# Performance work log

Measured on AMD Instinct MI355X. Metric: run time of the kernel, lower is better.

Reference implementation:

```python
import jax, jax.numpy as jnp
import numpy as np

N_NODES = 100000
N_EDGES = 1600000
IN_CH = 128
HID = 128
OUT_CH = 10
NUM_LAYERS = 3
NUM_GRAPHS = 512


def _glorot(key, shape):
    fan_in, fan_out = shape[0], shape[1]
    lim = jnp.sqrt(6.0 / (fan_in + fan_out))
    return jax.random.uniform(key, shape, jnp.float32, -lim, lim)


def setup_inputs() -> dict:
    key = jax.random.key(0)
    ks = jax.random.split(key, 20)
    inp = {}
    inp["x"] = jax.random.normal(ks[0], (N_NODES, IN_CH), jnp.float32)
    inp["edge_index"] = jax.random.randint(ks[1], (2, N_EDGES), 0, N_NODES, jnp.int64)
    inp["batch"] = jnp.sort(jax.random.randint(ks[2], (N_NODES,), 0, NUM_GRAPHS, jnp.int64))
    # GIN layer MLP params: Linear(in, hid) -> ReLU -> Linear(hid, hid)
    kidx = 3
    for l in range(NUM_LAYERS):
        d_in = IN_CH if l == 0 else HID
        inp[f"w1_{l}"] = _glorot(ks[kidx], (d_in, HID)); kidx += 1
        inp[f"b1_{l}"] = jnp.zeros((HID,), jnp.float32)
        inp[f"w2_{l}"] = _glorot(ks[kidx], (HID, HID)); kidx += 1
        inp[f"b2_{l}"] = jnp.zeros((HID,), jnp.float32)
    inp["lin_w"] = _glorot(ks[kidx], (HID, OUT_CH))
    inp["lin_b"] = jnp.zeros((OUT_CH,), jnp.float32)
    return inp


def _gin_forward(x, src, dst, batch, layer_params, lin_w, lin_b):
    h = x
    n_layers = len(layer_params)
    for i, (w1, b1, w2, b2) in enumerate(layer_params):
        # GINConv: (1 + eps) * h + sum_{j in N(i)} h_j, eps = 0
        agg = jax.ops.segment_sum(h[src], dst, num_segments=N_NODES)
        z = h + agg
        # MLP: Linear -> ReLU -> Linear
        h = jnp.maximum(z @ w1 + b1, 0.0) @ w2 + b2
        if i < n_layers - 1:  # inter-layer ReLU (PyG BasicGNN act)
            h = jnp.maximum(h, 0.0)
    # global_add_pool over batch ids -> [NUM_GRAPHS, HID]
    pooled = jax.ops.segment_sum(h, batch, num_segments=NUM_GRAPHS)
    # dropout(p=0.5) is identity in eval mode
    return pooled @ lin_w + lin_b


def reference(x, edge_index, batch,
              w1_0, b1_0, w2_0, b2_0,
              w1_1, b1_1, w2_1, b2_1,
              w1_2, b1_2, w2_2, b2_2,
              lin_w, lin_b):
    src, dst = edge_index[0], edge_index[1]
    layer_params = [(w1_0, b1_0, w2_0, b2_0),
                    (w1_1, b1_1, w2_1, b2_1),
                    (w1_2, b1_2, w2_2, b2_2)]
    return _gin_forward(x, src, dst, batch, layer_params, lin_w, lin_b)
```

## Files before the change

### kernel.cpp

```cpp
#include <hip/hip_runtime.h>

#define CH 128
#define OUTC 10
#define NB 256
#define BCAP 10240
#define PCHUNK 2048
#define PROWS 128

typedef __attribute__((ext_vector_type(8))) short short8;
typedef __attribute__((ext_vector_type(4))) float f32x4;


__device__ inline unsigned short f2bf(float f) {
    unsigned u = __builtin_bit_cast(unsigned, f);
    u += 0x7fffu + ((u >> 16) & 1u);
    return (unsigned short)(u >> 16);
}
__device__ inline float bflo(unsigned u) { return __builtin_bit_cast(float, u << 16); }
__device__ inline float bfhi(unsigned u) { return __builtin_bit_cast(float, u & 0xffff0000u); }

__device__ inline void acc8(float* a, const uint4& v) {
    a[0] += bflo(v.x); a[1] += bfhi(v.x);
    a[2] += bflo(v.y); a[3] += bfhi(v.y);
    a[4] += bflo(v.z); a[5] += bfhi(v.z);
    a[6] += bflo(v.w); a[7] += bfhi(v.w);
}


__global__ void convert_x_kernel(const float4* __restrict__ x4, uint2* __restrict__ xb, int n4) {
    int i = blockIdx.x * 256 + threadIdx.x;
    if (i < n4) {
        float4 v = x4[i];
        uint2 o;
        o.x = (unsigned)f2bf(v.x) | ((unsigned)f2bf(v.y) << 16);
        o.y = (unsigned)f2bf(v.z) | ((unsigned)f2bf(v.w) << 16);
        xb[i] = o;
    }
}


struct WPtrs { const float* s[6]; unsigned short* d[6]; };

__global__ void transpose_w_kernel(WPtrs p) {
    int m = blockIdx.y;
    int i = blockIdx.x * 256 + threadIdx.x;
    int k = i >> 7;
    int nn = i & 127;
    p.d[m][nn * CH + k] = f2bf(p.s[m][i]);
}


__global__ void partition_kernel(const int* __restrict__ src, const int* __restrict__ dst,
                                 int* __restrict__ bucketCnt, unsigned* __restrict__ pairs, int E) {
    __shared__ int hist[NB];
    __shared__ int base[NB];
    __shared__ int cur[NB];
    int tid = threadIdx.x;
    int e0 = blockIdx.x * PCHUNK;

    hist[tid] = 0;
    __syncthreads();
    #pragma unroll
    for (int i = 0; i < PCHUNK / 256; ++i) {
        int e = e0 + tid + i * 256;
        if (e < E) atomicAdd(&hist[dst[e] >> 9], 1);
    }
    __syncthreads();
    {
        int c = hist[tid];
        base[tid] = (c > 0) ? atomicAdd(&bucketCnt[tid], c) : 0;
        cur[tid] = 0;
    }
    __syncthreads();
    #pragma unroll
    for (int i = 0; i < PCHUNK / 256; ++i) {
        int e = e0 + tid + i * 256;
        if (e < E) {
            int d = dst[e];
            int bkt = d >> 9;
            int p = base[bkt] + atomicAdd(&cur[bkt], 1);
            if (p < BCAP)
                pairs[bkt * BCAP + p] = ((unsigned)(d & 511) << 17) | (unsigned)src[e];
        }
    }
}

__global__ void scan_buckets_kernel(const int* __restrict__ cnt, int* __restrict__ base) {
    __shared__ int sm[NB];
    int tid = threadIdx.x;
    sm[tid] = cnt[tid];
    __syncthreads();
    for (int off = 1; off < NB; off <<= 1) {
        int t = (tid >= off) ? sm[tid - off] : 0;
        __syncthreads();
        sm[tid] += t;
        __syncthreads();
    }
    base[tid] = sm[tid] - cnt[tid];
}


__launch_bounds__(256)
__global__ void build_csr_kernel(const unsigned* __restrict__ pairs, const int* __restrict__ bucketCnt,
                                 const int* __restrict__ bucketBase,
                                 int* __restrict__ offs, int* __restrict__ csr, int N) {
    __shared__ int ldeg[512];
    __shared__ int s0[512], s1[512];
    __shared__ int lexc[512];
    __shared__ int lcur[512];
    __shared__ int lcsr[BCAP];

    int b = blockIdx.x;
    int node0 = b << 9;
    if (node0 >= N) return;
    int nLocal = min(512, N - node0);
    int cnt = min(bucketCnt[b], BCAP);
    int gbase = bucketBase[b];
    int tid = threadIdx.x;

    for (int i = tid; i < 512; i += 256) ldeg[i] = 0;
    __syncthreads();
    for (int i = tid; i < cnt; i += 256)
        atomicAdd(&ldeg[pairs[b * BCAP + i] >> 17], 1);
    __syncthreads();

    for (int i = tid; i < 512; i += 256) s0[i] = ldeg[i];
    __syncthreads();
    int* sp = s0; int* dp = s1;
    for (int off = 1; off < 512; off <<= 1) {
        for (int i = tid; i < 512; i += 256)
            dp[i] = sp[i] + ((i >= off) ? sp[i - off] : 0);
        __syncthreads();
        int* t = sp; sp = dp; dp = t;
    }
    for (int i = tid; i < 512; i += 256) {
        int ex = sp[i] - ldeg[i];
        lexc[i] = ex;
        lcur[i] = ex;
    }
    __syncthreads();

    for (int i = tid; i < cnt; i += 256) {
        unsigned w = pairs[b * BCAP + i];
        int p = atomicAdd(&lcur[w >> 17], 1);
        lcsr[p] = (int)(w & 0x1ffffu);
    }
    __syncthreads();

    for (int i = tid; i < cnt; i += 256) csr[gbase + i] = lcsr[i];
    for (int i = tid; i < nLocal; i += 256) offs[node0 + i] = gbase + lexc[i];
    if (tid == 0 && node0 + nLocal == N) offs[N] = gbase + cnt;
}


template <int L>
__global__ void aggregate_kernel(const uint4* __restrict__ h4, const int* __restrict__ offs,
                                 const int* __restrict__ csr, uint4* __restrict__ z4, int n) {
    int node = blockIdx.x * 16 + (threadIdx.x >> 4);
    int lane = threadIdx.x & 15;
    if (node >= n) return;
    int beg = offs[node], end = offs[node + 1];

    float a[8];
    {
        uint4 self = h4[node * 16 + lane];
        a[0] = bflo(self.x); a[1] = bfhi(self.x);
        a[2] = bflo(self.y); a[3] = bfhi(self.y);
        a[4] = bflo(self.z); a[5] = bfhi(self.z);
        a[6] = bflo(self.w); a[7] = bfhi(self.w);
    }
    int e = beg;
    for (; e + 4 <= end; e += 4) {
        int s0 = csr[e], s1 = csr[e + 1], s2 = csr[e + 2], s3 = csr[e + 3];
        uint4 v0 = h4[s0 * 16 + lane];
        uint4 v1 = h4[s1 * 16 + lane];
        uint4 v2 = h4[s2 * 16 + lane];
        uint4 v3 = h4[s3 * 16 + lane];
        acc8(a, v0); acc8(a, v1); acc8(a, v2); acc8(a, v3);
    }
    for (; e < end; ++e) {
        uint4 v = h4[csr[e] * 16 + lane];
        acc8(a, v);
    }
    uint4 o;
    o.x = (unsigned)f2bf(a[0]) | ((unsigned)f2bf(a[1]) << 16);
    o.y = (unsigned)f2bf(a[2]) | ((unsigned)f2bf(a[3]) << 16);
    o.z = (unsigned)f2bf(a[4]) | ((unsigned)f2bf(a[5]) << 16);
    o.w = (unsigned)f2bf(a[6]) | ((unsigned)f2bf(a[7]) << 16);
    z4[node * 16 + lane] = o;
}


#define PQ 136
#define BM 128

template <int L>
__launch_bounds__(512, 2)
__global__ void mlp_mfma_kernel(const unsigned short* __restrict__ z,
                                const unsigned short* __restrict__ w1t, const float* __restrict__ b1,
                                const unsigned short* __restrict__ w2t, const float* __restrict__ b2,
                                unsigned short* __restrict__ hout, int n, int relu_out) {
    __shared__ __align__(16) unsigned short zs[BM * PQ];
    __shared__ __align__(16) unsigned short ws[CH * PQ];

    int tid = threadIdx.x;
    int row0 = blockIdx.x * BM;
    int wv = tid >> 6;
    int lane = tid & 63;
    int lm = lane & 15;
    int lq = lane >> 4;

    for (int i = tid; i < BM * 16; i += 512) {
        int r = i >> 4, c = i & 15;
        int row = row0 + r;
        uint4 v = (row < n) ? ((const uint4*)z)[row * 16 + c] : make_uint4(0, 0, 0, 0);
        *(uint4*)((char*)zs + r * (PQ * 2) + c * 16) = v;
    }
    for (int i = tid; i < CH * 16; i += 512) {
        int r = i >> 4, c = i & 15;
        *(uint4*)((char*)ws + r * (PQ * 2) + c * 16) = ((const uint4*)w1t)[i];
    }
    __syncthreads();

    f32x4 acc[8];
    #pragma unroll
    for (int nt = 0; nt < 8; ++nt) {
        float bv = b1[nt * 16 + lm];
        acc[nt] = (f32x4){bv, bv, bv, bv};
    }
    int arow = wv * 16 + lm;
    #pragma unroll
    for (int kb = 0; kb < CH; kb += 32) {
        short8 afr = *(const short8*)&zs[arow * PQ + kb + 8 * lq];
        #pragma unroll
        for (int nt = 0; nt < 8; ++nt) {
            short8 bfr = *(const short8*)&ws[(nt * 16 + lm) * PQ + kb + 8 * lq];
            acc[nt] = __builtin_amdgcn_mfma_f32_16x16x32_bf16(afr, bfr, acc[nt], 0, 0, 0);
        }
    }
    __syncthreads();

    #pragma unroll
    for (int nt = 0; nt < 8; ++nt)
        #pragma unroll
        for (int r = 0; r < 4; ++r) {
            float v = fmaxf(acc[nt][r], 0.f);
            zs[(wv * 16 + lq * 4 + r) * PQ + nt * 16 + lm] = f2bf(v);
        }
    for (int i = tid; i < CH * 16; i += 512) {
        int r = i >> 4, c = i & 15;
        *(uint4*)((char*)ws + r * (PQ * 2) + c * 16) = ((const uint4*)w2t)[i];
    }
    __syncthreads();

    #pragma unroll
    for (int nt = 0; nt < 8; ++nt) {
        float bv = b2[nt * 16 + lm];
        acc[nt] = (f32x4){bv, bv, bv, bv};
    }
    #pragma unroll
    for (int kb = 0; kb < CH; kb += 32) {
        short8 afr = *(const short8*)&zs[arow * PQ + kb + 8 * lq];
        #pragma unroll
        for (int nt = 0; nt < 8; ++nt) {
            short8 bfr = *(const short8*)&ws[(nt * 16 + lm) * PQ + kb + 8 * lq];
            acc[nt] = __builtin_amdgcn_mfma_f32_16x16x32_bf16(afr, bfr, acc[nt], 0, 0, 0);
        }
    }
    __syncthreads();

    #pragma unroll
    for (int nt = 0; nt < 8; ++nt)
        #pragma unroll
        for (int r = 0; r < 4; ++r) {
            float v = acc[nt][r];
            if (relu_out) v = fmaxf(v, 0.f);
            zs[(wv * 16 + lq * 4 + r) * PQ + nt * 16 + lm] = f2bf(v);
        }
    __syncthreads();

    for (int i = tid; i < BM * 16; i += 512) {
        int r = i >> 4, c = i & 15;
        int row = row0 + r;
        if (row < n)
            ((uint4*)hout)[row * 16 + c] = *(const uint4*)((char*)zs + r * (PQ * 2) + c * 16);
    }
}


__global__ void pool_partial_kernel(const unsigned* __restrict__ h2, const int* __restrict__ batch,
                                    float* __restrict__ pooled, int n) {
    int r0 = blockIdx.x * PROWS;
    int tid = threadIdx.x;
    int c2 = tid & 63;
    int rs = tid >> 6;
    float a0 = 0.f, a1 = 0.f;
    int prevg = -1;
    #pragma unroll 4
    for (int i = 0; i < PROWS / 4; ++i) {
        int r = r0 + rs + i * 4;
        if (r >= n) break;
        int g = batch[r];
        if (g != prevg) {
            if (prevg >= 0) {
                atomicAdd(&pooled[prevg * CH + 2 * c2], a0);
                atomicAdd(&pooled[prevg * CH + 2 * c2 + 1], a1);
            }
            prevg = g; a0 = 0.f; a1 = 0.f;
        }
        unsigned v = h2[r * 64 + c2];
        a0 += bflo(v); a1 += bfhi(v);
    }
    if (prevg >= 0) {
        atomicAdd(&pooled[prevg * CH + 2 * c2], a0);
        atomicAdd(&pooled[prevg * CH + 2 * c2 + 1], a1);
    }
}

__global__ void final_linear_kernel(const float* __restrict__ pooled, const float* __restrict__ lin_w,
                                    const float* __restrict__ lin_b, float* __restrict__ out) {
    int g = blockIdx.x;
    int tid = threadIdx.x;
    __shared__ float pl[CH];
    pl[tid] = pooled[g * CH + tid];
    __syncthreads();
    if (tid < OUTC) {
        float a = lin_b[tid];
        #pragma unroll 16
        for (int c = 0; c < CH; ++c) a = fmaf(pl[c], lin_w[c * OUTC + tid], a);
        out[g * OUTC + tid] = a;
    }
}


static inline size_t aln(size_t x) { return (x + 255) & ~size_t(255); }

extern "C" void kernel_launch(void* const* d_in, const int* in_sizes, int n_in,
                              void* d_out, int out_size, void* d_ws, size_t ws_size,
                              hipStream_t stream) {
    const float* x      = (const float*)d_in[0];
    const int*   ei     = (const int*)d_in[1];
    const int*   batch  = (const int*)d_in[2];
    const float* w1[3]  = {(const float*)d_in[3], (const float*)d_in[7],  (const float*)d_in[11]};
    const float* b1[3]  = {(const float*)d_in[4], (const float*)d_in[8],  (const float*)d_in[12]};
    const float* w2[3]  = {(const float*)d_in[5], (const float*)d_in[9],  (const float*)d_in[13]};
    const float* b2[3]  = {(const float*)d_in[6], (const float*)d_in[10], (const float*)d_in[14]};
    const float* lin_w  = (const float*)d_in[15];
    const float* lin_b  = (const float*)d_in[16];
    float* out = (float*)d_out;

    int E = in_sizes[1] / 2;
    int N = in_sizes[2];
    int n_graphs = out_size / OUTC;
    const int* src = ei;
    const int* dst = ei + E;

    char* p = (char*)d_ws;
    int* bucketCnt  = (int*)p; p += aln(NB * 4);
    int* bucketBase = (int*)p; p += aln(NB * 4);
    unsigned* pairs = (unsigned*)p; p += aln((size_t)NB * BCAP * 4);
    int* offs       = (int*)p; p += aln((size_t)(N + 1) * 4);
    int* csr        = (int*)p; p += aln((size_t)E * 4);
    unsigned short* xb = (unsigned short*)p; p += aln((size_t)N * CH * 2);
    unsigned short* zb = (unsigned short*)p; p += aln((size_t)N * CH * 2);
    unsigned short* hA = (unsigned short*)p; p += aln((size_t)N * CH * 2);
    unsigned short* hB = (unsigned short*)p; p += aln((size_t)N * CH * 2);
    float* pooled = (float*)p; p += aln((size_t)n_graphs * CH * 4);
    unsigned short* wt[6];
    for (int i = 0; i < 6; ++i) { wt[i] = (unsigned short*)p; p += aln((size_t)CH * CH * 2); }
    (void)ws_size; (void)n_in;

    convert_x_kernel<<<(N * CH / 4 + 255) / 256, 256, 0, stream>>>((const float4*)x, (uint2*)xb, N * CH / 4);
    WPtrs wp;
    for (int l = 0; l < 3; ++l) {
        wp.s[2 * l] = w1[l];     wp.d[2 * l] = wt[2 * l];
        wp.s[2 * l + 1] = w2[l]; wp.d[2 * l + 1] = wt[2 * l + 1];
    }
    transpose_w_kernel<<<dim3(64, 6), 256, 0, stream>>>(wp);

    hipMemsetAsync(bucketCnt, 0, NB * 4, stream);
    partition_kernel<<<(E + PCHUNK - 1) / PCHUNK, 256, 0, stream>>>(src, dst, bucketCnt, pairs, E);
    scan_buckets_kernel<<<1, NB, 0, stream>>>(bucketCnt, bucketBase);
    build_csr_kernel<<<NB, 256, 0, stream>>>(pairs, bucketCnt, bucketBase, offs, csr, N);

    int ablk = (N + 15) / 16;
    int mblk = (N + BM - 1) / BM;

    aggregate_kernel<0><<<ablk, 256, 0, stream>>>((const uint4*)xb, offs, csr, (uint4*)zb, N);
    mlp_mfma_kernel<0><<<mblk, 512, 0, stream>>>(zb, wt[0], b1[0], wt[1], b2[0], hA, N, 1);
    aggregate_kernel<1><<<ablk, 256, 0, stream>>>((const uint4*)hA, offs, csr, (uint4*)zb, N);
    mlp_mfma_kernel<1><<<mblk, 512, 0, stream>>>(zb, wt[2], b1[1], wt[3], b2[1], hB, N, 1);
    aggregate_kernel<2><<<ablk, 256, 0, stream>>>((const uint4*)hB, offs, csr, (uint4*)zb, N);
    mlp_mfma_kernel<2><<<mblk, 512, 0, stream>>>(zb, wt[4], b1[2], wt[5], b2[2], hA, N, 0);

    hipMemsetAsync(pooled, 0, (size_t)n_graphs * CH * 4, stream);
    pool_partial_kernel<<<(N + PROWS - 1) / PROWS, 256, 0, stream>>>(
        (const unsigned*)hA, batch, pooled, N);
    final_linear_kernel<<<n_graphs, CH, 0, stream>>>(pooled, lin_w, lin_b, out);
}
```

Before: 456.0 us.

## Fuse prep kernels, bucket scan into CSR build, pooling into last MLP

Merges the x conversion and weight transpose into one launch, folds the bucket prefix scan into every build_csr block, and fuses global add pooling into the final MLP kernel so the last hidden state is never written out or re-read. It also unrolls the aggregation gather loop to 8 neighbours with a 2-wide tail and adds launch bounds for occupancy. The aim is fewer kernel launches and less global memory traffic. The cost is a redundant 256-entry scan in each CSR block and possibly higher register pressure in the aggregate kernel.

```diff
diff --git a/kernel.cpp b/kernel.cpp
--- a/kernel.cpp
+++ b/kernel.cpp
@@ -5,7 +5,6 @@
 #define NB 256
 #define BCAP 10240
 #define PCHUNK 2048
-#define PROWS 128
 
 typedef __attribute__((ext_vector_type(8))) short short8;
 typedef __attribute__((ext_vector_type(4))) float f32x4;
@@ -27,26 +26,28 @@
 }
 
 
-__global__ void convert_x_kernel(const float4* __restrict__ x4, uint2* __restrict__ xb, int n4) {
-    int i = blockIdx.x * 256 + threadIdx.x;
-    if (i < n4) {
-        float4 v = x4[i];
-        uint2 o;
-        o.x = (unsigned)f2bf(v.x) | ((unsigned)f2bf(v.y) << 16);
-        o.y = (unsigned)f2bf(v.z) | ((unsigned)f2bf(v.w) << 16);
-        xb[i] = o;
-    }
-}
-
-
 struct WPtrs { const float* s[6]; unsigned short* d[6]; };
 
-__global__ void transpose_w_kernel(WPtrs p) {
-    int m = blockIdx.y;
-    int i = blockIdx.x * 256 + threadIdx.x;
-    int k = i >> 7;
-    int nn = i & 127;
-    p.d[m][nn * CH + k] = f2bf(p.s[m][i]);
+__global__ void prep_kernel(const float4* __restrict__ x4, uint2* __restrict__ xb, int n4,
+                            int nConvBlk, WPtrs p) {
+    int tid = threadIdx.x;
+    if ((int)blockIdx.x < nConvBlk) {
+        int i = blockIdx.x * 256 + tid;
+        if (i < n4) {
+            float4 v = x4[i];
+            uint2 o;
+            o.x = (unsigned)f2bf(v.x) | ((unsigned)f2bf(v.y) << 16);
+            o.y = (unsigned)f2bf(v.z) | ((unsigned)f2bf(v.w) << 16);
+            xb[i] = o;
+        }
+    } else {
+        int b = blockIdx.x - nConvBlk;
+        int m = b >> 6;
+        int i = (b & 63) * 256 + tid;
+        int k = i >> 7;
+        int nn = i & 127;
+        p.d[m][nn * CH + k] = f2bf(p.s[m][i]);
+    }
 }
 
 
@@ -85,25 +86,11 @@
     }
 }
 
-__global__ void scan_buckets_kernel(const int* __restrict__ cnt, int* __restrict__ base) {
-    __shared__ int sm[NB];
-    int tid = threadIdx.x;
-    sm[tid] = cnt[tid];
-    __syncthreads();
-    for (int off = 1; off < NB; off <<= 1) {
-        int t = (tid >= off) ? sm[tid - off] : 0;
-        __syncthreads();
-        sm[tid] += t;
-        __syncthreads();
-    }
-    base[tid] = sm[tid] - cnt[tid];
-}
-
 
 __launch_bounds__(256)
 __global__ void build_csr_kernel(const unsigned* __restrict__ pairs, const int* __restrict__ bucketCnt,
-                                 const int* __restrict__ bucketBase,
                                  int* __restrict__ offs, int* __restrict__ csr, int N) {
+    __shared__ int bsm[NB];
     __shared__ int ldeg[512];
     __shared__ int s0[512], s1[512];
     __shared__ int lexc[512];
@@ -114,9 +101,18 @@
     int node0 = b << 9;
     if (node0 >= N) return;
     int nLocal = min(512, N - node0);
+    int tid = threadIdx.x;
+
+    bsm[tid] = bucketCnt[tid];
+    __syncthreads();
+    for (int off = 1; off < NB; off <<= 1) {
+        int t = (tid >= off) ? bsm[tid - off] : 0;
+        __syncthreads();
+        bsm[tid] += t;
+        __syncthreads();
+    }
     int cnt = min(bucketCnt[b], BCAP);
-    int gbase = bucketBase[b];
-    int tid = threadIdx.x;
+    int gbase = bsm[b] - bucketCnt[b];
 
     for (int i = tid; i < 512; i += 256) ldeg[i] = 0;
     __syncthreads();
@@ -142,8 +138,8 @@
 
     for (int i = tid; i < cnt; i += 256) {
         unsigned w = pairs[b * BCAP + i];
-        int p = atomicAdd(&lcur[w >> 17], 1);
-        lcsr[p] = (int)(w & 0x1ffffu);
+        int ppos = atomicAdd(&lcur[w >> 17], 1);
+        lcsr[ppos] = (int)(w & 0x1ffffu);
     }
     __syncthreads();
 
@@ -154,6 +150,7 @@
 
 
 template <int L>
+__launch_bounds__(256, 8)
 __global__ void aggregate_kernel(const uint4* __restrict__ h4, const int* __restrict__ offs,
                                  const int* __restrict__ csr, uint4* __restrict__ z4, int n) {
     int node = blockIdx.x * 16 + (threadIdx.x >> 4);
@@ -170,15 +167,27 @@
         a[6] = bflo(self.w); a[7] = bfhi(self.w);
     }
     int e = beg;
-    for (; e + 4 <= end; e += 4) {
-        int s0 = csr[e], s1 = csr[e + 1], s2 = csr[e + 2], s3 = csr[e + 3];
+    for (; e + 8 <= end; e += 8) {
+        int s0 = csr[e],     s1 = csr[e + 1], s2 = csr[e + 2], s3 = csr[e + 3];
+        int s4 = csr[e + 4], s5 = csr[e + 5], s6 = csr[e + 6], s7 = csr[e + 7];
         uint4 v0 = h4[s0 * 16 + lane];
         uint4 v1 = h4[s1 * 16 + lane];
         uint4 v2 = h4[s2 * 16 + lane];
         uint4 v3 = h4[s3 * 16 + lane];
+        uint4 v4 = h4[s4 * 16 + lane];
+        uint4 v5 = h4[s5 * 16 + lane];
+        uint4 v6 = h4[s6 * 16 + lane];
+        uint4 v7 = h4[s7 * 16 + lane];
         acc8(a, v0); acc8(a, v1); acc8(a, v2); acc8(a, v3);
-    }
-    for (; e < end; ++e) {
+        acc8(a, v4); acc8(a, v5); acc8(a, v6); acc8(a, v7);
+    }
+    for (; e + 2 <= end; e += 2) {
+        int s0 = csr[e], s1 = csr[e + 1];
+        uint4 v0 = h4[s0 * 16 + lane];
+        uint4 v1 = h4[s1 * 16 + lane];
+        acc8(a, v0); acc8(a, v1);
+    }
+    if (e < end) {
         uint4 v = h4[csr[e] * 16 + lane];
         acc8(a, v);
     }
@@ -194,12 +203,14 @@
 #define PQ 136
 #define BM 128
 
-template <int L>
+template <int L, int RELU, int POOL>
 __launch_bounds__(512, 2)
 __global__ void mlp_mfma_kernel(const unsigned short* __restrict__ z,
                                 const unsigned short* __restrict__ w1t, const float* __restrict__ b1,
                                 const unsigned short* __restrict__ w2t, const float* __restrict__ b2,
-                                unsigned short* __restrict__ hout, int n, int relu_out) {
+                                unsigned short* __restrict__ hout,
+                                const int* __restrict__ batch, float* __restrict__ pooled,
+                                int n) {
     __shared__ __align__(16) unsigned short zs[BM * PQ];
     __shared__ __align__(16) unsigned short ws[CH * PQ];
 
@@ -274,48 +285,46 @@
         #pragma unroll
         for (int r = 0; r < 4; ++r) {
             float v = acc[nt][r];
-            if (relu_out) v = fmaxf(v, 0.f);
+            if (RELU) v = fmaxf(v, 0.f);
             zs[(wv * 16 + lq * 4 + r) * PQ + nt * 16 + lm] = f2bf(v);
         }
     __syncthreads();
 
-    for (int i = tid; i < BM * 16; i += 512) {
-        int r = i >> 4, c = i & 15;
-        int row = row0 + r;
-        if (row < n)
-            ((uint4*)hout)[row * 16 + c] = *(const uint4*)((char*)zs + r * (PQ * 2) + c * 16);
-    }
-}
-
-
-__global__ void pool_partial_kernel(const unsigned* __restrict__ h2, const int* __restrict__ batch,
-                                    float* __restrict__ pooled, int n) {
-    int r0 = blockIdx.x * PROWS;
-    int tid = threadIdx.x;
-    int c2 = tid & 63;
-    int rs = tid >> 6;
-    float a0 = 0.f, a1 = 0.f;
-    int prevg = -1;
-    #pragma unroll 4
-    for (int i = 0; i < PROWS / 4; ++i) {
-        int r = r0 + rs + i * 4;
-        if (r >= n) break;
-        int g = batch[r];
-        if (g != prevg) {
-            if (prevg >= 0) {
-                atomicAdd(&pooled[prevg * CH + 2 * c2], a0);
-                atomicAdd(&pooled[prevg * CH + 2 * c2 + 1], a1);
+    if (!POOL) {
+        for (int i = tid; i < BM * 16; i += 512) {
+            int r = i >> 4, c = i & 15;
+            int row = row0 + r;
+            if (row < n)
+                ((uint4*)hout)[row * 16 + c] = *(const uint4*)((char*)zs + r * (PQ * 2) + c * 16);
+        }
+    } else {
+        int c2 = tid & 63;
+        int rs = tid >> 6;
+        float a0 = 0.f, a1 = 0.f;
+        int prevg = -1;
+        #pragma unroll
+        for (int i = 0; i < BM / 8; ++i) {
+            int r = rs + 8 * i;
+            int row = row0 + r;
+            if (row >= n) break;
+            int g = batch[row];
+            if (g != prevg) {
+                if (prevg >= 0) {
+                    atomicAdd(&pooled[prevg * CH + 2 * c2], a0);
+                    atomicAdd(&pooled[prevg * CH + 2 * c2 + 1], a1);
+                }
+                prevg = g; a0 = 0.f; a1 = 0.f;
             }
-            prevg = g; a0 = 0.f; a1 = 0.f;
-        }
-        unsigned v = h2[r * 64 + c2];
-        a0 += bflo(v); a1 += bfhi(v);
-    }
-    if (prevg >= 0) {
-        atomicAdd(&pooled[prevg * CH + 2 * c2], a0);
-        atomicAdd(&pooled[prevg * CH + 2 * c2 + 1], a1);
-    }
-}
+            unsigned v = *(const unsigned*)((char*)zs + r * (PQ * 2) + c2 * 4);
+            a0 += bflo(v); a1 += bfhi(v);
+        }
+        if (prevg >= 0) {
+            atomicAdd(&pooled[prevg * CH + 2 * c2], a0);
+            atomicAdd(&pooled[prevg * CH + 2 * c2 + 1], a1);
+        }
+    }
+}
+
 
 __global__ void final_linear_kernel(const float* __restrict__ pooled, const float* __restrict__ lin_w,
                                     const float* __restrict__ lin_b, float* __restrict__ out) {
@@ -357,7 +366,6 @@
 
     char* p = (char*)d_ws;
     int* bucketCnt  = (int*)p; p += aln(NB * 4);
-    int* bucketBase = (int*)p; p += aln(NB * 4);
     unsigned* pairs = (unsigned*)p; p += aln((size_t)NB * BCAP * 4);
     int* offs       = (int*)p; p += aln((size_t)(N + 1) * 4);
     int* csr        = (int*)p; p += aln((size_t)E * 4);
@@ -370,31 +378,30 @@
     for (int i = 0; i < 6; ++i) { wt[i] = (unsigned short*)p; p += aln((size_t)CH * CH * 2); }
     (void)ws_size; (void)n_in;
 
-    convert_x_kernel<<<(N * CH / 4 + 255) / 256, 256, 0, stream>>>((const float4*)x, (uint2*)xb, N * CH / 4);
+    hipMemsetAsync(bucketCnt, 0, NB * 4, stream);
+    hipMemsetAsync(pooled, 0, (size_t)n_graphs * CH * 4, stream);
+
+    int n4 = N * CH / 4;
+    int nConvBlk = (n4 + 255) / 256;
     WPtrs wp;
     for (int l = 0; l < 3; ++l) {
         wp.s[2 * l] = w1[l];     wp.d[2 * l] = wt[2 * l];
         wp.s[2 * l + 1] = w2[l]; wp.d[2 * l + 1] = wt[2 * l + 1];
     }
-    transpose_w_kernel<<<dim3(64, 6), 256, 0, stream>>>(wp);
-
-    hipMemsetAsync(bucketCnt, 0, NB * 4, stream);
+    prep_kernel<<<nConvBlk + 384, 256, 0, stream>>>((const float4*)x, (uint2*)xb, n4, nConvBlk, wp);
+
     partition_kernel<<<(E + PCHUNK - 1) / PCHUNK, 256, 0, stream>>>(src, dst, bucketCnt, pairs, E);
-    scan_buckets_kernel<<<1, NB, 0, stream>>>(bucketCnt, bucketBase);
-    build_csr_kernel<<<NB, 256, 0, stream>>>(pairs, bucketCnt, bucketBase, offs, csr, N);
+    build_csr_kernel<<<NB, 256, 0, stream>>>(pairs, bucketCnt, offs, csr, N);
 
     int ablk = (N + 15) / 16;
     int mblk = (N + BM - 1) / BM;
 
     aggregate_kernel<0><<<ablk, 256, 0, stream>>>((const uint4*)xb, offs, csr, (uint4*)zb, N);
-    mlp_mfma_kernel<0><<<mblk, 512, 0, stream>>>(zb, wt[0], b1[0], wt[1], b2[0], hA, N, 1);
+    mlp_mfma_kernel<0, 1, 0><<<mblk, 512, 0, stream>>>(zb, wt[0], b1[0], wt[1], b2[0], hA, batch, pooled, N);
     aggregate_kernel<1><<<ablk, 256, 0, stream>>>((const uint4*)hA, offs, csr, (uint4*)zb, N);
-    mlp_mfma_kernel<1><<<mblk, 512, 0, stream>>>(zb, wt[2], b1[1], wt[3], b2[1], hB, N, 1);
+    mlp_mfma_kernel<1, 1, 0><<<mblk, 512, 0, stream>>>(zb, wt[2], b1[1], wt[3], b2[1], hB, batch, pooled, N);
     aggregate_kernel<2><<<ablk, 256, 0, stream>>>((const uint4*)hB, offs, csr, (uint4*)zb, N);
-    mlp_mfma_kernel<2><<<mblk, 512, 0, stream>>>(zb, wt[4], b1[2], wt[5], b2[2], hA, N, 0);
-
-    hipMemsetAsync(pooled, 0, (size_t)n_graphs * CH * 4, stream);
-    pool_partial_kernel<<<(N + PROWS - 1) / PROWS, 256, 0, stream>>>(
-        (const unsigned*)hA, batch, pooled, N);
+    mlp_mfma_kernel<2, 0, 1><<<mblk, 512, 0, stream>>>(zb, wt[4], b1[2], wt[5], b2[2], hA, batch, pooled, N);
+
     final_linear_kernel<<<n_graphs, CH, 0, stream>>>(pooled, lin_w, lin_b, out);
 }
```

Measured after the change: 625.6 us. 1.37x slower.
